# Optimization experiments

Hardware: AMD Instinct MI355X
Metric: run time of the kernel (lower is better)

Reference implementation:

```python
import jax, jax.numpy as jnp
import numpy as np

N = 50000
E = 800000
IN_DIM = 256
HID = 256
OUT_DIM = 2


def setup_inputs() -> dict:
    key = jax.random.key(0)
    ks = jax.random.split(key, 10)
    x = jax.random.normal(ks[0], (N, IN_DIM), dtype=jnp.float32)
    edge_index = jax.random.randint(ks[1], (2, E), 0, N, dtype=jnp.int64)
    # Glorot-ish scaling so activations stay well-conditioned through 4 layers
    def w(k, fan_in, fan_out):
        return jax.random.normal(k, (fan_in, fan_out), dtype=jnp.float32) / jnp.sqrt(jnp.float32(fan_in))
    return {
        "x": x,
        "edge_index": edge_index,
        "W0": w(ks[2], IN_DIM, HID), "b0": jnp.zeros((HID,), jnp.float32),
        "W1": w(ks[3], HID, HID),    "b1": jnp.zeros((HID,), jnp.float32),
        "W2": w(ks[4], HID, HID),    "b2": jnp.zeros((HID,), jnp.float32),
        "W3": w(ks[5], HID, OUT_DIM), "b3": jnp.zeros((OUT_DIM,), jnp.float32),
    }


def _gcn_norm(edge_index, n, dtype):
    # PyG gcn_norm with self-loops: deg over destination, norm = d^-1/2[src]*d^-1/2[dst]
    loops = jnp.arange(n, dtype=edge_index.dtype)
    src = jnp.concatenate([edge_index[0], loops])
    dst = jnp.concatenate([edge_index[1], loops])
    deg = jax.ops.segment_sum(jnp.ones_like(dst, dtype=dtype), dst, num_segments=n)
    dis = deg ** -0.5  # deg >= 1 due to self-loops
    norm = dis[src] * dis[dst]
    return src, dst, norm


def reference(x, edge_index, W0, b0, W1, b1, W2, b2, W3, b3):
    n = x.shape[0]
    src, dst, norm = _gcn_norm(edge_index, n, x.dtype)

    def conv(h, W, b):
        h = h @ W                              # [N, F_out] dense GEMM
        msg = h[src] * norm[:, None]           # edge-gather + scale
        agg = jax.ops.segment_sum(msg, dst, num_segments=n)  # scatter-add
        return agg + b

    h = jax.nn.relu(conv(x, W0, b0))
    h = jax.nn.relu(conv(h, W1, b1))
    h = jax.nn.relu(conv(h, W2, b2))
    return conv(h, W3, b3)
```

## Files before the change

### kernel.cpp

```cpp
#include <hip/hip_runtime.h>

#define N_NODES 50000
#define N_EDGES 800000

static inline int cdiv(int a, int b) { return (a + b - 1) / b; }

typedef __attribute__((ext_vector_type(8))) short bf16x8;
typedef __attribute__((ext_vector_type(4))) float f32x4;
typedef __attribute__((ext_vector_type(2))) float f32x2;
typedef __attribute__((ext_vector_type(4))) unsigned int u32x4;

static __device__ __forceinline__ unsigned short f2bf(float f) {
    unsigned int u = __float_as_uint(f);
    unsigned int r = (u + 0x7FFF + ((u >> 16) & 1)) >> 16;
    return (unsigned short)r;
}
static __device__ __forceinline__ float bf2f(unsigned short h) {
    return __uint_as_float((unsigned int)h << 16);
}
static __device__ __forceinline__ float bf_lo(unsigned int u) { return __uint_as_float(u << 16); }
static __device__ __forceinline__ float bf_hi(unsigned int u) { return __uint_as_float(u & 0xFFFF0000u); }

static __device__ __forceinline__ int logc(int p) {
    int pl = p & 63;
    return (p & ~63) + (pl & 3) * 16 + (pl >> 2);
}

static __device__ __forceinline__ int2 ldnt2(const int2* p) {
    unsigned long long u = __builtin_nontemporal_load((const unsigned long long*)p);
    int2 r;
    r.x = (int)(u & 0xFFFFFFFFull);
    r.y = (int)(u >> 32);
    return r;
}

static __device__ __forceinline__ void acc8p(f32x2* acc, uint4 v, float wgt) {
    f32x2 w2;
    w2.x = wgt;
    w2.y = wgt;
    f32x2 p;
    p.x = bf_lo(v.x); p.y = bf_hi(v.x); acc[0] += p * w2;
    p.x = bf_lo(v.y); p.y = bf_hi(v.y); acc[1] += p * w2;
    p.x = bf_lo(v.z); p.y = bf_hi(v.z); acc[2] += p * w2;
    p.x = bf_lo(v.w); p.y = bf_hi(v.w); acc[3] += p * w2;
}


__global__ void k_count(const int* __restrict__ edst, int* cnt, int e) {
    int i = (blockIdx.x * 256 + threadIdx.x) * 4;
    if (i + 3 < e) {
        int4 v = *(const int4*)(edst + i);
        atomicAdd(&cnt[v.x], 1);
        atomicAdd(&cnt[v.y], 1);
        atomicAdd(&cnt[v.z], 1);
        atomicAdd(&cnt[v.w], 1);
    } else {
        for (int k = i; k < e; ++k) atomicAdd(&cnt[edst[k]], 1);
    }
}

__global__ __launch_bounds__(256) void k_scan1(const int* __restrict__ cnt,
                                               int* __restrict__ row_ptr,
                                               float* __restrict__ dis,
                                               int* __restrict__ blk, int n) {
    __shared__ int sums[256];
    int t = threadIdx.x;
    int base = blockIdx.x * 1024 + t * 4;
    int c0 = 0, c1 = 0, c2 = 0, c3 = 0;
    if (base + 3 < n) {
        int4 v = *(const int4*)(cnt + base);
        c0 = v.x + 1; c1 = v.y + 1; c2 = v.z + 1; c3 = v.w + 1;
    } else {
        if (base + 0 < n) c0 = cnt[base + 0] + 1;
        if (base + 1 < n) c1 = cnt[base + 1] + 1;
        if (base + 2 < n) c2 = cnt[base + 2] + 1;
        if (base + 3 < n) c3 = cnt[base + 3] + 1;
    }
    int s = c0 + c1 + c2 + c3;
    sums[t] = s;
    __syncthreads();
    int x = s;
    for (int off = 1; off < 256; off <<= 1) {
        int y = (t >= off) ? sums[t - off] : 0;
        __syncthreads();
        x += y;
        sums[t] = x;
        __syncthreads();
    }
    int excl = x - s;
    if (base + 0 < n) { row_ptr[base + 0] = excl;                dis[base + 0] = rsqrtf((float)c0); }
    if (base + 1 < n) { row_ptr[base + 1] = excl + c0;           dis[base + 1] = rsqrtf((float)c1); }
    if (base + 2 < n) { row_ptr[base + 2] = excl + c0 + c1;      dis[base + 2] = rsqrtf((float)c2); }
    if (base + 3 < n) { row_ptr[base + 3] = excl + c0 + c1 + c2; dis[base + 3] = rsqrtf((float)c3); }
    if (t == 255) blk[blockIdx.x] = x;
}

__global__ __launch_bounds__(256) void k_scan2(int* __restrict__ blk,
                                               int* __restrict__ row_ptr_n, int nb) {
    __shared__ int sums[256];
    int t = threadIdx.x;
    int s = (t < nb) ? blk[t] : 0;
    sums[t] = s;
    __syncthreads();
    int x = s;
    for (int off = 1; off < 256; off <<= 1) {
        int y = (t >= off) ? sums[t - off] : 0;
        __syncthreads();
        x += y;
        sums[t] = x;
        __syncthreads();
    }
    if (t < nb) blk[t] = x - s;
    if (t == 255) row_ptr_n[0] = x;
}

__global__ __launch_bounds__(256) void k_scan3(int* __restrict__ row_ptr,
                                               int* __restrict__ pos,
                                               const int* __restrict__ blk, int n) {
    int base = blockIdx.x * 1024 + threadIdx.x * 4;
    int off = blk[blockIdx.x];
#pragma unroll
    for (int i = 0; i < 4; ++i) {
        int idx = base + i;
        if (idx < n) {
            int v = row_ptr[idx] + off;
            row_ptr[idx] = v;
            pos[idx] = v;
        }
    }
}

__global__ void k_fill(const int* __restrict__ esrc, const int* __restrict__ edst,
                       int* pos, const float* __restrict__ dis,
                       int2* __restrict__ eg, int e, int n) {
    int i = blockIdx.x * 256 + threadIdx.x;
    if (i < e) {
        int s = esrc[i], d = edst[i];
        int p = atomicAdd(&pos[d], 1);
        unsigned long long u = (unsigned long long)(unsigned int)s |
                               ((unsigned long long)(unsigned int)__float_as_int(dis[s] * dis[d]) << 32);
        __builtin_nontemporal_store(u, (unsigned long long*)&eg[p]);
    } else if (i < e + n) {
        int v = i - e;
        int p = atomicAdd(&pos[v], 1);
        float dv = dis[v];
        unsigned long long u = (unsigned long long)(unsigned int)v |
                               ((unsigned long long)(unsigned int)__float_as_int(dv * dv) << 32);
        __builtin_nontemporal_store(u, (unsigned long long*)&eg[p]);
    }
}


__global__ __launch_bounds__(256) void k_prep(const float* __restrict__ W0,
                                              const float* __restrict__ W1,
                                              const float* __restrict__ W2,
                                              const float* __restrict__ b0,
                                              const float* __restrict__ b1,
                                              const float* __restrict__ b2,
                                              const float* __restrict__ W3,
                                              unsigned short* __restrict__ Wth,
                                              unsigned short* __restrict__ Wtl,
                                              float* __restrict__ bpw,
                                              const float* __restrict__ X,
                                              unsigned short* __restrict__ Xh, long total4) {
    if (blockIdx.x < 768) {
        int layer = blockIdx.x >> 8;
        int n = blockIdx.x & 255;
        int p = threadIdx.x;
        const float* W = layer == 0 ? W0 : (layer == 1 ? W1 : W2);
        int k = (layer != 0) ? logc(p) : p;
        float v = W[(size_t)k * 256 + n];
        unsigned short h = f2bf(v);
        size_t o = (size_t)layer * 65536 + (size_t)n * 256 + p;
        Wth[o] = h;
        Wtl[o] = f2bf(v - bf2f(h));
    } else if (blockIdx.x == 768) {
        int p = threadIdx.x;
        int c = logc(p);
        bpw[p] = b0[c];
        bpw[256 + p] = b1[c];
        bpw[512 + p] = b2[c];
        bpw[768 + p * 2 + 0] = W3[(size_t)c * 2 + 0];
        bpw[768 + p * 2 + 1] = W3[(size_t)c * 2 + 1];
    } else {
        long i = (long)(blockIdx.x - 769) * 256 + threadIdx.x;
        if (i >= total4) return;
        float4 v = *(const float4*)(X + i * 4);
        ushort4 h;
        h.x = f2bf(v.x);
        h.y = f2bf(v.y);
        h.z = f2bf(v.z);
        h.w = f2bf(v.w);
        *(ushort4*)(Xh + i * 4) = h;
    }
}


#define GEMM_RB 196

__global__ __launch_bounds__(256) void k_gemm_mfma(const unsigned short* __restrict__ Ah,
                                                   const unsigned short* __restrict__ Wth,
                                                   const unsigned short* __restrict__ Wtl,
                                                   unsigned short* __restrict__ C, int M) {
    __shared__ unsigned short Wh[64][264];
    __shared__ unsigned short Wl[64][136];
    int rowblk = blockIdx.x % GEMM_RB;
    int colblk = blockIdx.x / GEMM_RB;
    int c0 = colblk * 64;
    int m0 = rowblk * 256;
    int t = threadIdx.x;
    int sr = t >> 2;

    {
        int hk0 = (t & 3) * 64;
        const unsigned short* gh = Wth + (size_t)(c0 + sr) * 256 + hk0;
        unsigned short* lh = &Wh[sr][hk0];
#pragma unroll
        for (int i = 0; i < 8; ++i)
            *(uint4*)(lh + i * 8) = *(const uint4*)(gh + i * 8);
        int lk0 = (t & 3) * 32;
        const unsigned short* gl = Wtl + (size_t)(c0 + sr) * 256 + lk0;
        unsigned short* ll = &Wl[sr][lk0];
#pragma unroll
        for (int i = 0; i < 4; ++i)
            *(uint4*)(ll + i * 8) = *(const uint4*)(gl + i * 8);
    }
    __syncthreads();

    int lane = t & 63, wave = t >> 6;
    int quad = lane >> 4, l16 = lane & 15;

    const unsigned short* aph[4];
#pragma unroll
    for (int mt = 0; mt < 4; ++mt) {
        int m = m0 + wave * 64 + mt * 16 + l16;
        if (m >= M) m = M - 1;
        aph[mt] = Ah + (size_t)m * 256 + quad * 8;
    }

    f32x4 acc[4][4];
#pragma unroll
    for (int i = 0; i < 4; ++i)
#pragma unroll
        for (int j = 0; j < 4; ++j) acc[i][j] = (f32x4){0.f, 0.f, 0.f, 0.f};

#pragma unroll 2
    for (int kc = 0; kc < 4; ++kc) {
        int ko = kc * 32;
        bf16x8 ahf[4];
#pragma unroll
        for (int mt = 0; mt < 4; ++mt) ahf[mt] = *(const bf16x8*)(aph[mt] + ko);
#pragma unroll
        for (int nt = 0; nt < 4; ++nt) {
            bf16x8 bh = *(const bf16x8*)&Wh[nt * 16 + l16][ko + quad * 8];
            bf16x8 bl = *(const bf16x8*)&Wl[nt * 16 + l16][ko + quad * 8];
#pragma unroll
            for (int mt = 0; mt < 4; ++mt) {
                acc[mt][nt] = __builtin_amdgcn_mfma_f32_16x16x32_bf16(ahf[mt], bh, acc[mt][nt], 0, 0, 0);
                acc[mt][nt] = __builtin_amdgcn_mfma_f32_16x16x32_bf16(ahf[mt], bl, acc[mt][nt], 0, 0, 0);
            }
        }
    }

    __syncthreads();
    {
        int lk0 = (t & 3) * 32;
        const unsigned short* gl = Wtl + (size_t)(c0 + sr) * 256 + 128 + lk0;
        unsigned short* ll = &Wl[sr][lk0];
#pragma unroll
        for (int i = 0; i < 4; ++i)
            *(uint4*)(ll + i * 8) = *(const uint4*)(gl + i * 8);
    }
    __syncthreads();

#pragma unroll 2
    for (int kc = 4; kc < 8; ++kc) {
        int ko = kc * 32;
        int kol = ko - 128;
        bf16x8 ahf[4];
#pragma unroll
        for (int mt = 0; mt < 4; ++mt) ahf[mt] = *(const bf16x8*)(aph[mt] + ko);
#pragma unroll
        for (int nt = 0; nt < 4; ++nt) {
            bf16x8 bh = *(const bf16x8*)&Wh[nt * 16 + l16][ko + quad * 8];
            bf16x8 bl = *(const bf16x8*)&Wl[nt * 16 + l16][kol + quad * 8];
#pragma unroll
            for (int mt = 0; mt < 4; ++mt) {
                acc[mt][nt] = __builtin_amdgcn_mfma_f32_16x16x32_bf16(ahf[mt], bh, acc[mt][nt], 0, 0, 0);
                acc[mt][nt] = __builtin_amdgcn_mfma_f32_16x16x32_bf16(ahf[mt], bl, acc[mt][nt], 0, 0, 0);
            }
        }
    }

#pragma unroll
    for (int mt = 0; mt < 4; ++mt) {
#pragma unroll
        for (int r = 0; r < 4; ++r) {
            int row = m0 + wave * 64 + mt * 16 + quad * 4 + r;
            if (row < M) {
                ushort4 sv;
                sv.x = f2bf(acc[mt][0][r]);
                sv.y = f2bf(acc[mt][1][r]);
                sv.z = f2bf(acc[mt][2][r]);
                sv.w = f2bf(acc[mt][3][r]);
                *(ushort4*)(C + (size_t)row * 256 + c0 + l16 * 4) = sv;
            }
        }
    }
}


template <int MODE>
__global__ __launch_bounds__(256, 8) void k_agg256(const unsigned short* __restrict__ t,
                                                   const int* __restrict__ row_ptr,
                                                   const int2* __restrict__ eg,
                                                   const float* __restrict__ bp,
                                                   unsigned short* __restrict__ outh,
                                                   const float* __restrict__ w3p,
                                                   float* __restrict__ t2, int n) {
    int lane = threadIdx.x & 63;
    int wave = threadIdx.x >> 6;
    int node = blockIdx.x * 4 + wave;
    if (node >= n) return;
    int half = lane >> 5;
    int fl = lane & 31;
    int beg = row_ptr[node], end = row_ptr[node + 1];
    f32x2 acc2[4];
#pragma unroll
    for (int i = 0; i < 4; ++i) { acc2[i].x = 0.f; acc2[i].y = 0.f; }
    const unsigned short* tp = t + fl * 8;

    int e = beg + half;
    for (; e + 10 < end; e += 12) {
        int2 a0 = ldnt2(eg + e), a1 = ldnt2(eg + e + 2), a2 = ldnt2(eg + e + 4);
        int2 a3 = ldnt2(eg + e + 6), a4 = ldnt2(eg + e + 8), a5 = ldnt2(eg + e + 10);
        uint4 v0 = *(const uint4*)(tp + (size_t)a0.x * 256);
        uint4 v1 = *(const uint4*)(tp + (size_t)a1.x * 256);
        uint4 v2 = *(const uint4*)(tp + (size_t)a2.x * 256);
        uint4 v3 = *(const uint4*)(tp + (size_t)a3.x * 256);
        uint4 v4 = *(const uint4*)(tp + (size_t)a4.x * 256);
        uint4 v5 = *(const uint4*)(tp + (size_t)a5.x * 256);
        acc8p(acc2, v0, __int_as_float(a0.y));
        acc8p(acc2, v1, __int_as_float(a1.y));
        acc8p(acc2, v2, __int_as_float(a2.y));
        acc8p(acc2, v3, __int_as_float(a3.y));
        acc8p(acc2, v4, __int_as_float(a4.y));
        acc8p(acc2, v5, __int_as_float(a5.y));
    }
    for (; e + 6 < end; e += 8) {
        int2 a0 = ldnt2(eg + e), a1 = ldnt2(eg + e + 2);
        int2 a2 = ldnt2(eg + e + 4), a3 = ldnt2(eg + e + 6);
        uint4 v0 = *(const uint4*)(tp + (size_t)a0.x * 256);
        uint4 v1 = *(const uint4*)(tp + (size_t)a1.x * 256);
        uint4 v2 = *(const uint4*)(tp + (size_t)a2.x * 256);
        uint4 v3 = *(const uint4*)(tp + (size_t)a3.x * 256);
        acc8p(acc2, v0, __int_as_float(a0.y));
        acc8p(acc2, v1, __int_as_float(a1.y));
        acc8p(acc2, v2, __int_as_float(a2.y));
        acc8p(acc2, v3, __int_as_float(a3.y));
    }
    for (; e + 2 < end; e += 4) {
        int2 a0 = ldnt2(eg + e), a1 = ldnt2(eg + e + 2);
        uint4 v0 = *(const uint4*)(tp + (size_t)a0.x * 256);
        uint4 v1 = *(const uint4*)(tp + (size_t)a1.x * 256);
        acc8p(acc2, v0, __int_as_float(a0.y));
        acc8p(acc2, v1, __int_as_float(a1.y));
    }
    if (e < end) {
        int2 a0 = ldnt2(eg + e);
        uint4 v0 = *(const uint4*)(tp + (size_t)a0.x * 256);
        acc8p(acc2, v0, __int_as_float(a0.y));
    }

    float va[8];
#pragma unroll
    for (int i = 0; i < 4; ++i) { va[2 * i] = acc2[i].x; va[2 * i + 1] = acc2[i].y; }
#pragma unroll
    for (int i = 0; i < 8; ++i) va[i] += __shfl_xor(va[i], 32);

    if (MODE == 0) {
        if (half == 0) {
            float4 bA = *(const float4*)(bp + fl * 8);
            float4 bB = *(const float4*)(bp + fl * 8 + 4);
            float r0 = fmaxf(va[0] + bA.x, 0.f), r1 = fmaxf(va[1] + bA.y, 0.f);
            float r2 = fmaxf(va[2] + bA.z, 0.f), r3 = fmaxf(va[3] + bA.w, 0.f);
            float r4 = fmaxf(va[4] + bB.x, 0.f), r5 = fmaxf(va[5] + bB.y, 0.f);
            float r6 = fmaxf(va[6] + bB.z, 0.f), r7 = fmaxf(va[7] + bB.w, 0.f);
            u32x4 w;
            w.x = (unsigned)f2bf(r0) | ((unsigned)f2bf(r1) << 16);
            w.y = (unsigned)f2bf(r2) | ((unsigned)f2bf(r3) << 16);
            w.z = (unsigned)f2bf(r4) | ((unsigned)f2bf(r5) << 16);
            w.w = (unsigned)f2bf(r6) | ((unsigned)f2bf(r7) << 16);
            __builtin_nontemporal_store(w, (u32x4*)(outh + (size_t)node * 256 + fl * 8));
        }
    } else {
        float4 bA = *(const float4*)(bp + fl * 8);
        float4 bB = *(const float4*)(bp + fl * 8 + 4);
        float r0 = fmaxf(va[0] + bA.x, 0.f), r1 = fmaxf(va[1] + bA.y, 0.f);
        float r2 = fmaxf(va[2] + bA.z, 0.f), r3 = fmaxf(va[3] + bA.w, 0.f);
        float r4 = fmaxf(va[4] + bB.x, 0.f), r5 = fmaxf(va[5] + bB.y, 0.f);
        float r6 = fmaxf(va[6] + bB.z, 0.f), r7 = fmaxf(va[7] + bB.w, 0.f);
        const float* wp = w3p + fl * 16;
        float4 wA = *(const float4*)(wp + 0);
        float4 wB = *(const float4*)(wp + 4);
        float4 wC = *(const float4*)(wp + 8);
        float4 wD = *(const float4*)(wp + 12);
        float s0 = r0 * wA.x + r1 * wA.z + r2 * wB.x + r3 * wB.z +
                   r4 * wC.x + r5 * wC.z + r6 * wD.x + r7 * wD.z;
        float s1 = r0 * wA.y + r1 * wA.w + r2 * wB.y + r3 * wB.w +
                   r4 * wC.y + r5 * wC.w + r6 * wD.y + r7 * wD.w;
#pragma unroll
        for (int off = 16; off > 0; off >>= 1) {
            s0 += __shfl_xor(s0, off);
            s1 += __shfl_xor(s1, off);
        }
        if (lane == 0) {
            f32x2 o;
            o.x = s0;
            o.y = s1;
            __builtin_nontemporal_store(o, (f32x2*)(t2 + (size_t)node * 2));
        }
    }
}


__global__ void k_agg2(const float* __restrict__ t2,
                       const int* __restrict__ row_ptr,
                       const int2* __restrict__ eg,
                       const float* __restrict__ b3,
                       float* __restrict__ out, int n) {
    int tid = blockIdx.x * 256 + threadIdx.x;
    int node = tid >> 2;
    int sub = tid & 3;
    if (node >= n) return;
    int beg = row_ptr[node], end = row_ptr[node + 1];
    float a0 = 0.f, a1 = 0.f;
    for (int e = beg + sub; e < end; e += 4) {
        int2 m = ldnt2(eg + e);
        float w = __int_as_float(m.y);
        float2 v = *(const float2*)(t2 + (size_t)m.x * 2);
        a0 += w * v.x;
        a1 += w * v.y;
    }
    a0 += __shfl_xor(a0, 1); a1 += __shfl_xor(a1, 1);
    a0 += __shfl_xor(a0, 2); a1 += __shfl_xor(a1, 2);
    if (sub == 0) {
        out[(size_t)node * 2 + 0] = a0 + b3[0];
        out[(size_t)node * 2 + 1] = a1 + b3[1];
    }
}


extern "C" void kernel_launch(void* const* d_in, const int* in_sizes, int n_in,
                              void* d_out, int out_size, void* d_ws, size_t ws_size,
                              hipStream_t stream) {
    const int N = N_NODES, E = N_EDGES;
    const float* x  = (const float*)d_in[0];
    const int* ei   = (const int*)d_in[1];
    const int* esrc = ei;
    const int* edst = ei + E;
    const float* W0 = (const float*)d_in[2];
    const float* b0 = (const float*)d_in[3];
    const float* W1 = (const float*)d_in[4];
    const float* b1 = (const float*)d_in[5];
    const float* W2 = (const float*)d_in[6];
    const float* b2 = (const float*)d_in[7];
    const float* W3 = (const float*)d_in[8];
    const float* b3 = (const float*)d_in[9];
    float* out = (float*)d_out;

    unsigned short* Ahh = (unsigned short*)d_ws;
    unsigned short* Tb  = Ahh + (size_t)N * 256;
    unsigned short* Wth = Tb + (size_t)N * 256;
    unsigned short* Wtl = Wth + 3 * 65536;
    int2*  eg     = (int2*)(Wtl + 3 * 65536);
    float* t2     = (float*)(eg + (E + N));
    float* bpw    = t2 + (size_t)N * 2;
    float* dis    = bpw + 1280;
    int*   cnt    = (int*)(dis + N);
    int*   row_ptr= cnt + N;
    int*   pos    = row_ptr + (N + 1);
    int*   blk    = pos + N;

    const int NB = cdiv(N, 1024);

    hipMemsetAsync(cnt, 0, (size_t)N * sizeof(int), stream);
    k_count<<<cdiv(E, 1024), 256, 0, stream>>>(edst, cnt, E);
    k_scan1<<<NB, 256, 0, stream>>>(cnt, row_ptr, dis, blk, N);
    k_scan2<<<1, 256, 0, stream>>>(blk, row_ptr + N, NB);
    k_scan3<<<NB, 256, 0, stream>>>(row_ptr, pos, blk, N);
    k_fill<<<cdiv(E + N, 256), 256, 0, stream>>>(esrc, edst, pos, dis, eg, E, N);

    const int ggrid = GEMM_RB * 4;
    const int agrid = cdiv(N, 4);
    const long total4 = (long)N * 64;
    const int CA = cdiv((int)total4, 256);

    k_prep<<<769 + CA, 256, 0, stream>>>(W0, W1, W2, b0, b1, b2, W3, Wth, Wtl, bpw, x, Ahh, total4);

    k_gemm_mfma<<<ggrid, 256, 0, stream>>>(Ahh, Wth, Wtl, Tb, N);
    k_agg256<0><<<agrid, 256, 0, stream>>>(Tb, row_ptr, eg, bpw, Ahh, nullptr, nullptr, N);
    k_gemm_mfma<<<ggrid, 256, 0, stream>>>(Ahh, Wth + 65536, Wtl + 65536, Tb, N);
    k_agg256<0><<<agrid, 256, 0, stream>>>(Tb, row_ptr, eg, bpw + 256, Ahh, nullptr, nullptr, N);
    k_gemm_mfma<<<ggrid, 256, 0, stream>>>(Ahh, Wth + 2 * 65536, Wtl + 2 * 65536, Tb, N);
    k_agg256<1><<<agrid, 256, 0, stream>>>(Tb, row_ptr, eg, bpw + 512, nullptr, bpw + 768, t2, N);
    k_agg2<<<cdiv(4 * N, 256), 256, 0, stream>>>(t2, row_ptr, eg, b3, out, N);
}
```

Baseline: 465.8 us.

## Read low-part weights from global in GEMM and use grid-stride aggregation

The GEMM kernel no longer stages the low-part weight split (Wtl) in shared memory. Each lane now loads its bf16 fragment straight from global memory, which removes the mid-kernel reload and two barriers and merges the two K-halves into one loop. LDS use drops, and launch bounds of 4 ask for more resident blocks. The aggregation kernel becomes a grid-stride loop over nodes with a fixed grid of 2048 blocks instead of one wave per node. The cost is more global/L2 traffic for the weight fragments, and possibly worse load balance or latency hiding in aggregation.

```diff
diff --git a/kernel.cpp b/kernel.cpp
--- a/kernel.cpp
+++ b/kernel.cpp
@@ -198,12 +198,11 @@
 
 #define GEMM_RB 196
 
-__global__ __launch_bounds__(256) void k_gemm_mfma(const unsigned short* __restrict__ Ah,
-                                                   const unsigned short* __restrict__ Wth,
-                                                   const unsigned short* __restrict__ Wtl,
-                                                   unsigned short* __restrict__ C, int M) {
+__global__ __launch_bounds__(256, 4) void k_gemm_mfma(const unsigned short* __restrict__ Ah,
+                                                      const unsigned short* __restrict__ Wth,
+                                                      const unsigned short* __restrict__ Wtl,
+                                                      unsigned short* __restrict__ C, int M) {
     __shared__ unsigned short Wh[64][264];
-    __shared__ unsigned short Wl[64][136];
     int rowblk = blockIdx.x % GEMM_RB;
     int colblk = blockIdx.x / GEMM_RB;
     int c0 = colblk * 64;
@@ -218,12 +217,6 @@
 #pragma unroll
         for (int i = 0; i < 8; ++i)
             *(uint4*)(lh + i * 8) = *(const uint4*)(gh + i * 8);
-        int lk0 = (t & 3) * 32;
-        const unsigned short* gl = Wtl + (size_t)(c0 + sr) * 256 + lk0;
-        unsigned short* ll = &Wl[sr][lk0];
-#pragma unroll
-        for (int i = 0; i < 4; ++i)
-            *(uint4*)(ll + i * 8) = *(const uint4*)(gl + i * 8);
     }
     __syncthreads();
 
@@ -237,6 +230,7 @@
         if (m >= M) m = M - 1;
         aph[mt] = Ah + (size_t)m * 256 + quad * 8;
     }
+    const unsigned short* blp = Wtl + (size_t)(c0 + l16) * 256 + quad * 8;
 
     f32x4 acc[4][4];
 #pragma unroll
@@ -245,7 +239,7 @@
         for (int j = 0; j < 4; ++j) acc[i][j] = (f32x4){0.f, 0.f, 0.f, 0.f};
 
 #pragma unroll 2
-    for (int kc = 0; kc < 4; ++kc) {
+    for (int kc = 0; kc < 8; ++kc) {
         int ko = kc * 32;
         bf16x8 ahf[4];
 #pragma unroll
@@ -253,37 +247,7 @@
 #pragma unroll
         for (int nt = 0; nt < 4; ++nt) {
             bf16x8 bh = *(const bf16x8*)&Wh[nt * 16 + l16][ko + quad * 8];
-            bf16x8 bl = *(const bf16x8*)&Wl[nt * 16 + l16][ko + quad * 8];
-#pragma unroll
-            for (int mt = 0; mt < 4; ++mt) {
-                acc[mt][nt] = __builtin_amdgcn_mfma_f32_16x16x32_bf16(ahf[mt], bh, acc[mt][nt], 0, 0, 0);
-                acc[mt][nt] = __builtin_amdgcn_mfma_f32_16x16x32_bf16(ahf[mt], bl, acc[mt][nt], 0, 0, 0);
-            }
-        }
-    }
-
-    __syncthreads();
-    {
-        int lk0 = (t & 3) * 32;
-        const unsigned short* gl = Wtl + (size_t)(c0 + sr) * 256 + 128 + lk0;
-        unsigned short* ll = &Wl[sr][lk0];
-#pragma unroll
-        for (int i = 0; i < 4; ++i)
-            *(uint4*)(ll + i * 8) = *(const uint4*)(gl + i * 8);
-    }
-    __syncthreads();
-
-#pragma unroll 2
-    for (int kc = 4; kc < 8; ++kc) {
-        int ko = kc * 32;
-        int kol = ko - 128;
-        bf16x8 ahf[4];
-#pragma unroll
-        for (int mt = 0; mt < 4; ++mt) ahf[mt] = *(const bf16x8*)(aph[mt] + ko);
-#pragma unroll
-        for (int nt = 0; nt < 4; ++nt) {
-            bf16x8 bh = *(const bf16x8*)&Wh[nt * 16 + l16][ko + quad * 8];
-            bf16x8 bl = *(const bf16x8*)&Wl[nt * 16 + l16][kol + quad * 8];
+            bf16x8 bl = *(const bf16x8*)(blp + nt * 16 * 256 + ko);
 #pragma unroll
             for (int mt = 0; mt < 4; ++mt) {
                 acc[mt][nt] = __builtin_amdgcn_mfma_f32_16x16x32_bf16(ahf[mt], bh, acc[mt][nt], 0, 0, 0);
@@ -320,105 +284,107 @@
                                                    float* __restrict__ t2, int n) {
     int lane = threadIdx.x & 63;
     int wave = threadIdx.x >> 6;
-    int node = blockIdx.x * 4 + wave;
-    if (node >= n) return;
     int half = lane >> 5;
     int fl = lane & 31;
-    int beg = row_ptr[node], end = row_ptr[node + 1];
-    f32x2 acc2[4];
-#pragma unroll
-    for (int i = 0; i < 4; ++i) { acc2[i].x = 0.f; acc2[i].y = 0.f; }
     const unsigned short* tp = t + fl * 8;
-
-    int e = beg + half;
-    for (; e + 10 < end; e += 12) {
-        int2 a0 = ldnt2(eg + e), a1 = ldnt2(eg + e + 2), a2 = ldnt2(eg + e + 4);
-        int2 a3 = ldnt2(eg + e + 6), a4 = ldnt2(eg + e + 8), a5 = ldnt2(eg + e + 10);
-        uint4 v0 = *(const uint4*)(tp + (size_t)a0.x * 256);
-        uint4 v1 = *(const uint4*)(tp + (size_t)a1.x * 256);
-        uint4 v2 = *(const uint4*)(tp + (size_t)a2.x * 256);
-        uint4 v3 = *(const uint4*)(tp + (size_t)a3.x * 256);
-        uint4 v4 = *(const uint4*)(tp + (size_t)a4.x * 256);
-        uint4 v5 = *(const uint4*)(tp + (size_t)a5.x * 256);
-        acc8p(acc2, v0, __int_as_float(a0.y));
-        acc8p(acc2, v1, __int_as_float(a1.y));
-        acc8p(acc2, v2, __int_as_float(a2.y));
-        acc8p(acc2, v3, __int_as_float(a3.y));
-        acc8p(acc2, v4, __int_as_float(a4.y));
-        acc8p(acc2, v5, __int_as_float(a5.y));
-    }
-    for (; e + 6 < end; e += 8) {
-        int2 a0 = ldnt2(eg + e), a1 = ldnt2(eg + e + 2);
-        int2 a2 = ldnt2(eg + e + 4), a3 = ldnt2(eg + e + 6);
-        uint4 v0 = *(const uint4*)(tp + (size_t)a0.x * 256);
-        uint4 v1 = *(const uint4*)(tp + (size_t)a1.x * 256);
-        uint4 v2 = *(const uint4*)(tp + (size_t)a2.x * 256);
-        uint4 v3 = *(const uint4*)(tp + (size_t)a3.x * 256);
-        acc8p(acc2, v0, __int_as_float(a0.y));
-        acc8p(acc2, v1, __int_as_float(a1.y));
-        acc8p(acc2, v2, __int_as_float(a2.y));
-        acc8p(acc2, v3, __int_as_float(a3.y));
-    }
-    for (; e + 2 < end; e += 4) {
-        int2 a0 = ldnt2(eg + e), a1 = ldnt2(eg + e + 2);
-        uint4 v0 = *(const uint4*)(tp + (size_t)a0.x * 256);
-        uint4 v1 = *(const uint4*)(tp + (size_t)a1.x * 256);
-        acc8p(acc2, v0, __int_as_float(a0.y));
-        acc8p(acc2, v1, __int_as_float(a1.y));
-    }
-    if (e < end) {
-        int2 a0 = ldnt2(eg + e);
-        uint4 v0 = *(const uint4*)(tp + (size_t)a0.x * 256);
-        acc8p(acc2, v0, __int_as_float(a0.y));
-    }
-
-    float va[8];
-#pragma unroll
-    for (int i = 0; i < 4; ++i) { va[2 * i] = acc2[i].x; va[2 * i + 1] = acc2[i].y; }
-#pragma unroll
-    for (int i = 0; i < 8; ++i) va[i] += __shfl_xor(va[i], 32);
-
-    if (MODE == 0) {
-        if (half == 0) {
+    int stride = gridDim.x * 4;
+
+    for (int node = blockIdx.x * 4 + wave; node < n; node += stride) {
+        int beg = row_ptr[node], end = row_ptr[node + 1];
+        f32x2 acc2[4];
+#pragma unroll
+        for (int i = 0; i < 4; ++i) { acc2[i].x = 0.f; acc2[i].y = 0.f; }
+
+        int e = beg + half;
+        for (; e + 10 < end; e += 12) {
+            int2 a0 = ldnt2(eg + e), a1 = ldnt2(eg + e + 2), a2 = ldnt2(eg + e + 4);
+            int2 a3 = ldnt2(eg + e + 6), a4 = ldnt2(eg + e + 8), a5 = ldnt2(eg + e + 10);
+            uint4 v0 = *(const uint4*)(tp + (size_t)a0.x * 256);
+            uint4 v1 = *(const uint4*)(tp + (size_t)a1.x * 256);
+            uint4 v2 = *(const uint4*)(tp + (size_t)a2.x * 256);
+            uint4 v3 = *(const uint4*)(tp + (size_t)a3.x * 256);
+            uint4 v4 = *(const uint4*)(tp + (size_t)a4.x * 256);
+            uint4 v5 = *(const uint4*)(tp + (size_t)a5.x * 256);
+            acc8p(acc2, v0, __int_as_float(a0.y));
+            acc8p(acc2, v1, __int_as_float(a1.y));
+            acc8p(acc2, v2, __int_as_float(a2.y));
+            acc8p(acc2, v3, __int_as_float(a3.y));
+            acc8p(acc2, v4, __int_as_float(a4.y));
+            acc8p(acc2, v5, __int_as_float(a5.y));
+        }
+        for (; e + 6 < end; e += 8) {
+            int2 a0 = ldnt2(eg + e), a1 = ldnt2(eg + e + 2);
+            int2 a2 = ldnt2(eg + e + 4), a3 = ldnt2(eg + e + 6);
+            uint4 v0 = *(const uint4*)(tp + (size_t)a0.x * 256);
+            uint4 v1 = *(const uint4*)(tp + (size_t)a1.x * 256);
+            uint4 v2 = *(const uint4*)(tp + (size_t)a2.x * 256);
+            uint4 v3 = *(const uint4*)(tp + (size_t)a3.x * 256);
+            acc8p(acc2, v0, __int_as_float(a0.y));
+            acc8p(acc2, v1, __int_as_float(a1.y));
+            acc8p(acc2, v2, __int_as_float(a2.y));
+            acc8p(acc2, v3, __int_as_float(a3.y));
+        }
+        for (; e + 2 < end; e += 4) {
+            int2 a0 = ldnt2(eg + e), a1 = ldnt2(eg + e + 2);
+            uint4 v0 = *(const uint4*)(tp + (size_t)a0.x * 256);
+            uint4 v1 = *(const uint4*)(tp + (size_t)a1.x * 256);
+            acc8p(acc2, v0, __int_as_float(a0.y));
+            acc8p(acc2, v1, __int_as_float(a1.y));
+        }
+        if (e < end) {
+            int2 a0 = ldnt2(eg + e);
+            uint4 v0 = *(const uint4*)(tp + (size_t)a0.x * 256);
+            acc8p(acc2, v0, __int_as_float(a0.y));
+        }
+
+        float va[8];
+#pragma unroll
+        for (int i = 0; i < 4; ++i) { va[2 * i] = acc2[i].x; va[2 * i + 1] = acc2[i].y; }
+#pragma unroll
+        for (int i = 0; i < 8; ++i) va[i] += __shfl_xor(va[i], 32);
+
+        if (MODE == 0) {
+            if (half == 0) {
+                float4 bA = *(const float4*)(bp + fl * 8);
+                float4 bB = *(const float4*)(bp + fl * 8 + 4);
+                float r0 = fmaxf(va[0] + bA.x, 0.f), r1 = fmaxf(va[1] + bA.y, 0.f);
+                float r2 = fmaxf(va[2] + bA.z, 0.f), r3 = fmaxf(va[3] + bA.w, 0.f);
+                float r4 = fmaxf(va[4] + bB.x, 0.f), r5 = fmaxf(va[5] + bB.y, 0.f);
+                float r6 = fmaxf(va[6] + bB.z, 0.f), r7 = fmaxf(va[7] + bB.w, 0.f);
+                u32x4 w;
+                w.x = (unsigned)f2bf(r0) | ((unsigned)f2bf(r1) << 16);
+                w.y = (unsigned)f2bf(r2) | ((unsigned)f2bf(r3) << 16);
+                w.z = (unsigned)f2bf(r4) | ((unsigned)f2bf(r5) << 16);
+                w.w = (unsigned)f2bf(r6) | ((unsigned)f2bf(r7) << 16);
+                __builtin_nontemporal_store(w, (u32x4*)(outh + (size_t)node * 256 + fl * 8));
+            }
+        } else {
             float4 bA = *(const float4*)(bp + fl * 8);
             float4 bB = *(const float4*)(bp + fl * 8 + 4);
             float r0 = fmaxf(va[0] + bA.x, 0.f), r1 = fmaxf(va[1] + bA.y, 0.f);
             float r2 = fmaxf(va[2] + bA.z, 0.f), r3 = fmaxf(va[3] + bA.w, 0.f);
             float r4 = fmaxf(va[4] + bB.x, 0.f), r5 = fmaxf(va[5] + bB.y, 0.f);
             float r6 = fmaxf(va[6] + bB.z, 0.f), r7 = fmaxf(va[7] + bB.w, 0.f);
-            u32x4 w;
-            w.x = (unsigned)f2bf(r0) | ((unsigned)f2bf(r1) << 16);
-            w.y = (unsigned)f2bf(r2) | ((unsigned)f2bf(r3) << 16);
-            w.z = (unsigned)f2bf(r4) | ((unsigned)f2bf(r5) << 16);
-            w.w = (unsigned)f2bf(r6) | ((unsigned)f2bf(r7) << 16);
-            __builtin_nontemporal_store(w, (u32x4*)(outh + (size_t)node * 256 + fl * 8));
-        }
-    } else {
-        float4 bA = *(const float4*)(bp + fl * 8);
-        float4 bB = *(const float4*)(bp + fl * 8 + 4);
-        float r0 = fmaxf(va[0] + bA.x, 0.f), r1 = fmaxf(va[1] + bA.y, 0.f);
-        float r2 = fmaxf(va[2] + bA.z, 0.f), r3 = fmaxf(va[3] + bA.w, 0.f);
-        float r4 = fmaxf(va[4] + bB.x, 0.f), r5 = fmaxf(va[5] + bB.y, 0.f);
-        float r6 = fmaxf(va[6] + bB.z, 0.f), r7 = fmaxf(va[7] + bB.w, 0.f);
-        const float* wp = w3p + fl * 16;
-        float4 wA = *(const float4*)(wp + 0);
-        float4 wB = *(const float4*)(wp + 4);
-        float4 wC = *(const float4*)(wp + 8);
-        float4 wD = *(const float4*)(wp + 12);
-        float s0 = r0 * wA.x + r1 * wA.z + r2 * wB.x + r3 * wB.z +
-                   r4 * wC.x + r5 * wC.z + r6 * wD.x + r7 * wD.z;
-        float s1 = r0 * wA.y + r1 * wA.w + r2 * wB.y + r3 * wB.w +
-                   r4 * wC.y + r5 * wC.w + r6 * wD.y + r7 * wD.w;
-#pragma unroll
-        for (int off = 16; off > 0; off >>= 1) {
-            s0 += __shfl_xor(s0, off);
-            s1 += __shfl_xor(s1, off);
-        }
-        if (lane == 0) {
-            f32x2 o;
-            o.x = s0;
-            o.y = s1;
-            __builtin_nontemporal_store(o, (f32x2*)(t2 + (size_t)node * 2));
+            const float* wp = w3p + fl * 16;
+            float4 wA = *(const float4*)(wp + 0);
+            float4 wB = *(const float4*)(wp + 4);
+            float4 wC = *(const float4*)(wp + 8);
+            float4 wD = *(const float4*)(wp + 12);
+            float s0 = r0 * wA.x + r1 * wA.z + r2 * wB.x + r3 * wB.z +
+                       r4 * wC.x + r5 * wC.z + r6 * wD.x + r7 * wD.z;
+            float s1 = r0 * wA.y + r1 * wA.w + r2 * wB.y + r3 * wB.w +
+                       r4 * wC.y + r5 * wC.w + r6 * wD.y + r7 * wD.w;
+#pragma unroll
+            for (int off = 16; off > 0; off >>= 1) {
+                s0 += __shfl_xor(s0, off);
+                s1 += __shfl_xor(s1, off);
+            }
+            if (lane == 0) {
+                f32x2 o;
+                o.x = s0;
+                o.y = s1;
+                __builtin_nontemporal_store(o, (f32x2*)(t2 + (size_t)node * 2));
+            }
         }
     }
 }
@@ -492,7 +458,7 @@
     k_fill<<<cdiv(E + N, 256), 256, 0, stream>>>(esrc, edst, pos, dis, eg, E, N);
 
     const int ggrid = GEMM_RB * 4;
-    const int agrid = cdiv(N, 4);
+    const int agrid = 2048;
     const long total4 = (long)N * 64;
     const int CA = cdiv((int)total4, 256);
 
```

Result: slower. 568.8 us (+22.1%).
